# Kernel tuning notes

Measured on AMD Instinct MI355X. Metric: run time of the kernel, lower is better.

Reference implementation:

```python
import jax, jax.numpy as jnp
import numpy as np
import math

B, N, DQ, DK, DV, H = 8, 1024, 512, 512, 512, 8


def setup_inputs() -> dict:
    key = jax.random.key(0)
    ks = jax.random.split(key, 9)
    s = 0.02
    return {
        "Q": jax.random.normal(ks[0], (B, N, DQ), jnp.float32),
        "K": jax.random.normal(ks[1], (B, N, DK), jnp.float32),
        "mask": jax.random.bernoulli(ks[2], 0.9, (B, N)).astype(jnp.float32),
        "Wq": jax.random.normal(ks[3], (DQ, DV), jnp.float32) * s,
        "bq": jnp.zeros((DV,), jnp.float32),
        "Wk": jax.random.normal(ks[4], (DK, DV), jnp.float32) * s,
        "bk": jnp.zeros((DV,), jnp.float32),
        "Wv": jax.random.normal(ks[5], (DK, DV), jnp.float32) * s,
        "bv": jnp.zeros((DV,), jnp.float32),
        "Wo": jax.random.normal(ks[6], (DV, DV), jnp.float32) * s,
        "bo": jnp.zeros((DV,), jnp.float32),
    }


def reference(Q, K, mask, Wq, bq, Wk, bk, Wv, bv, Wo, bo):
    b, n, _ = Q.shape
    dV = Wq.shape[1]
    dh = dV // H
    scale = 1.0 / math.sqrt(dV)
    m = mask[..., None]                      # [B,N,1]
    Qp = (Q @ Wq + bq) * m                   # [B,N,dV]
    Kp = (K @ Wk + bk) * m
    Vp = (K @ Wv + bv) * m
    # torch.cat(x.split(dh,2),0) == head-major stacking -> keep as [H,B,N,dh]
    q = Qp.reshape(b, n, H, dh).transpose(2, 0, 1, 3)
    k = Kp.reshape(b, n, H, dh).transpose(2, 0, 1, 3)
    v = Vp.reshape(b, n, H, dh).transpose(2, 0, 1, 3)
    S = jnp.einsum('hbnd,hbmd->hbnm', q, k) * scale   # [H,B,N,N]
    mx = jnp.max(S, axis=3, keepdims=True)            # unmasked row max (faithful)
    m1 = mask[None, :, :, None]                       # [1,B,N,1]
    m2 = mask[None, :, None, :]                       # [1,B,1,N]
    num = jnp.exp((S - mx) * m1 * m2) * m1 * m2
    A = num / (jnp.sum(num, axis=3, keepdims=True) + 1e-16)
    O = q + jnp.einsum('hbnm,hbmd->hbnd', A, v)       # residual on Q_
    O = O.transpose(1, 2, 0, 3).reshape(b, n, dV)     # un-split heads
    O = O + jax.nn.relu((O @ Wo + bo) * m)
    return O
```

## Files before the change

kernel.cpp:

```cpp
#include <hip/hip_runtime.h>

typedef short bf16x8 __attribute__((ext_vector_type(8)));
typedef float f32x4 __attribute__((ext_vector_type(4)));

#define MFMA16(a, b, c) __builtin_amdgcn_mfma_f32_16x16x32_bf16((a), (b), (c), 0, 0, 0)

#define GLOAD_LDS16(g, l)                                              \
  __builtin_amdgcn_global_load_lds(                                    \
      (const __attribute__((address_space(1))) unsigned int*)(g),      \
      (__attribute__((address_space(3))) unsigned int*)(l), 16, 0, 0)

__device__ __forceinline__ unsigned short f2b(float f) {
  union { float f; unsigned int u; } x; x.f = f;
  unsigned int r = x.u + 0x7FFFu + ((x.u >> 16) & 1u);
  return (unsigned short)(r >> 16);
}
__device__ __forceinline__ float b2f(unsigned short h) {
  union { unsigned int u; float f; } x; x.u = ((unsigned int)h) << 16;
  return x.f;
}
__device__ __forceinline__ unsigned int cvtpk(float lo, float hi) {
  unsigned int r;
  asm("v_cvt_pk_bf16_f32 %0, %1, %2" : "=v"(r) : "v"(lo), "v"(hi));
  return r;
}

__global__ __launch_bounds__(256) void wtrans_kernel(
    const float* __restrict__ Wq, const float* __restrict__ Wk,
    const float* __restrict__ Wv, const float* __restrict__ Wo,
    short* __restrict__ Wt) {
  __shared__ float tile[64][65];
  const int z = blockIdx.z;
  const float* W = (z == 0) ? Wq : (z == 1) ? Wk : (z == 2) ? Wv : Wo;
  const int k0 = blockIdx.x * 64, n0 = blockIdx.y * 64;
  const int t = threadIdx.x;
  const int r = t >> 4, cc = (t & 15) * 4;
#pragma unroll
  for (int it = 0; it < 4; ++it) {
    int row = r + it * 16;
    const float4 v = *(const float4*)(W + (k0 + row) * 512 + n0 + cc);
    tile[row][cc + 0] = v.x; tile[row][cc + 1] = v.y;
    tile[row][cc + 2] = v.z; tile[row][cc + 3] = v.w;
  }
  __syncthreads();
  short* out = Wt + z * (512 * 512);
#pragma unroll
  for (int it = 0; it < 4; ++it) {
    int nrow = r + it * 16;
    unsigned int u0 = cvtpk(tile[cc + 0][nrow], tile[cc + 1][nrow]);
    unsigned int u1 = cvtpk(tile[cc + 2][nrow], tile[cc + 3][nrow]);
    uint2 uv; uv.x = u0; uv.y = u1;
    *(uint2*)(out + (n0 + nrow) * 512 + k0 + cc) = uv;
  }
}

__global__ __launch_bounds__(256) void cvt_kernel(
    const float* __restrict__ Q, const float* __restrict__ K,
    const float* __restrict__ mask,
    short* __restrict__ Qb, short* __restrict__ Kb, float* __restrict__ ml) {
  if (blockIdx.y == 0 && blockIdx.x < 4) {
    int i = (blockIdx.x * 256 + threadIdx.x) * 8;
    float4 a = *(const float4*)(mask + i);
    float4 bb = *(const float4*)(mask + i + 4);
    float4 ra, rb;
    ra.x = (a.x != 0.f) ? 0.f : -1e30f;
    ra.y = (a.y != 0.f) ? 0.f : -1e30f;
    ra.z = (a.z != 0.f) ? 0.f : -1e30f;
    ra.w = (a.w != 0.f) ? 0.f : -1e30f;
    rb.x = (bb.x != 0.f) ? 0.f : -1e30f;
    rb.y = (bb.y != 0.f) ? 0.f : -1e30f;
    rb.z = (bb.z != 0.f) ? 0.f : -1e30f;
    rb.w = (bb.w != 0.f) ? 0.f : -1e30f;
    *(float4*)(ml + i) = ra;
    *(float4*)(ml + i + 4) = rb;
  }
  const float* src = blockIdx.y ? K : Q;
  short* dst = blockIdx.y ? Kb : Qb;
  int i = (blockIdx.x * 256 + threadIdx.x) * 8;
  float4 v0 = *(const float4*)(src + i);
  float4 v1 = *(const float4*)(src + i + 4);
  uint2 a, b;
  a.x = cvtpk(v0.x, v0.y); a.y = cvtpk(v0.z, v0.w);
  b.x = cvtpk(v1.x, v1.y); b.y = cvtpk(v1.z, v1.w);
  *(uint2*)(dst + i) = a;
  *(uint2*)(dst + i + 4) = b;
}

__device__ __forceinline__ void gemm_bf16_core(
    const short* __restrict__ A, const short* __restrict__ Wt,
    short* Al, short* Bl, int m0, int t, f32x4 acc[4][4]) {
  const int lane = t & 63, w = t >> 6;
  const int c = lane & 15, g = lane >> 4;
  const int wr = w >> 1, wc = w & 1;
  const int lr = lane >> 3;
  const int sswz = ((lane & 7) ^ lr) << 3;
  const int swc = (c & 7) << 3;

  auto STAGE = [&](int kt, int buf) {
    short* Ad = Al + buf * 8192;
    short* Bd = Bl + buf * 8192;
#pragma unroll
    for (int it = 0; it < 4; ++it) {
      int row = w * 32 + it * 8;
      GLOAD_LDS16(A + (size_t)(m0 + row + lr) * 512 + kt * 64 + sswz, Ad + row * 64);
      GLOAD_LDS16(Wt + (size_t)(row + lr) * 512 + kt * 64 + sswz, Bd + row * 64);
    }
  };

  STAGE(0, 0);
  STAGE(1, 1);

  for (int kt = 0; kt < 8; ++kt) {
    if (kt < 7) { asm volatile("s_waitcnt vmcnt(8)" ::: "memory"); }
    else        { asm volatile("s_waitcnt vmcnt(0)" ::: "memory"); }
    __builtin_amdgcn_s_barrier();
    __builtin_amdgcn_sched_barrier(0);
    const short* Ac = Al + (kt & 1) * 8192;
    const short* Bc = Bl + (kt & 1) * 8192;
    __builtin_amdgcn_s_setprio(1);
#pragma unroll
    for (int kc = 0; kc < 2; ++kc) {
      bf16x8 af[4], bfr[4];
#pragma unroll
      for (int mi = 0; mi < 4; ++mi) {
        int r = wr * 64 + mi * 16 + c;
        af[mi] = *(const bf16x8*)(Ac + r * 64 + ((kc * 32 + 8 * g) ^ swc));
      }
#pragma unroll
      for (int ni = 0; ni < 4; ++ni) {
        int r = wc * 64 + ni * 16 + c;
        bfr[ni] = *(const bf16x8*)(Bc + r * 64 + ((kc * 32 + 8 * g) ^ swc));
      }
#pragma unroll
      for (int mi = 0; mi < 4; ++mi)
#pragma unroll
        for (int ni = 0; ni < 4; ++ni)
          acc[mi][ni] = MFMA16(af[mi], bfr[ni], acc[mi][ni]);
    }
    __builtin_amdgcn_s_setprio(0);
    __builtin_amdgcn_sched_barrier(0);
    __builtin_amdgcn_s_barrier();
    __builtin_amdgcn_sched_barrier(0);
    if (kt < 6) STAGE(kt + 2, kt & 1);
  }
}

__global__ __launch_bounds__(256) void proj2_kernel(
    const short* __restrict__ Qb, const short* __restrict__ Kb,
    const short* __restrict__ Wt4,
    const float* __restrict__ bq, const float* __restrict__ bk, const float* __restrict__ bv,
    const float* __restrict__ maskf,
    short* __restrict__ Qp, short* __restrict__ Kp, short* __restrict__ Vt) {
  __shared__ short Al[2 * 128 * 64];
  __shared__ short Bl[2 * 128 * 64];
  const int by = blockIdx.y;
  const int m0 = blockIdx.x * 128;
  const int t = threadIdx.x;
  const short* A;
  const short* Wt;
  const float* bias;
  int nbase;
  if (by < 4) { A = Qb; nbase = by * 128; Wt = Wt4 + nbase * 512; bias = bq; }
  else if (by < 8) { A = Kb; nbase = (by - 4) * 128; Wt = Wt4 + 262144 + nbase * 512; bias = bk; }
  else { A = Kb; nbase = (by - 8) * 128; Wt = Wt4 + 524288 + nbase * 512; bias = bv; }

  const f32x4 zz = {0.f, 0.f, 0.f, 0.f};
  f32x4 acc[4][4];
#pragma unroll
  for (int mi = 0; mi < 4; ++mi)
#pragma unroll
    for (int ni = 0; ni < 4; ++ni) acc[mi][ni] = zz;
  gemm_bf16_core(A, Wt, Al, Bl, m0, t, acc);

  const int lane = t & 63, w = t >> 6;
  const int c = lane & 15, g = lane >> 4;
  const int wr = w >> 1, wc = w & 1;
  float mk[4][4];
#pragma unroll
  for (int mi = 0; mi < 4; ++mi) {
    int mbase = m0 + wr * 64 + mi * 16 + 4 * g;
#pragma unroll
    for (int i = 0; i < 4; ++i) mk[mi][i] = maskf[mbase + i];
  }
  if (by < 8) {
    short* out = (by < 4) ? Qp : Kp;
#pragma unroll
    for (int ni = 0; ni < 4; ++ni) {
      int n = nbase + wc * 64 + ni * 16 + c;
      float bval = bias[n];
#pragma unroll
      for (int mi = 0; mi < 4; ++mi) {
        int mbase = m0 + wr * 64 + mi * 16 + 4 * g;
#pragma unroll
        for (int i = 0; i < 4; ++i)
          out[(size_t)(mbase + i) * 512 + n] = (short)f2b((acc[mi][ni][i] + bval) * mk[mi][i]);
      }
    }
  } else {
#pragma unroll
    for (int ni = 0; ni < 4; ++ni) {
      int d = nbase + wc * 64 + ni * 16 + c;
      int h = d >> 6, dd = d & 63;
      float bval = bias[d];
#pragma unroll
      for (int mi = 0; mi < 4; ++mi) {
        int mbase = m0 + wr * 64 + mi * 16 + 4 * g;
        int bi = mbase >> 10, seq0 = mbase & 1023;
        unsigned int u0 = cvtpk((acc[mi][ni][0] + bval) * mk[mi][0],
                                (acc[mi][ni][1] + bval) * mk[mi][1]);
        unsigned int u1 = cvtpk((acc[mi][ni][2] + bval) * mk[mi][2],
                                (acc[mi][ni][3] + bval) * mk[mi][3]);
        uint2 uv; uv.x = u0; uv.y = u1;
        *(uint2*)(Vt + ((size_t)(bi * 8 + h) * 64 + dd) * 1024 + seq0) = uv;
      }
    }
  }
}

__global__ __launch_bounds__(256) void attn_kernel(
    const short* __restrict__ Qp, const short* __restrict__ Kp,
    const short* __restrict__ Vt, const float* __restrict__ mask,
    const float* __restrict__ ml,
    float* __restrict__ Ob, short* __restrict__ Obb) {
  __shared__ short Kl[2][64][64];
  __shared__ short Vl[2][64][64];
  __shared__ short Pl[4][16][64];
  __shared__ float Mlds[1024];
  const int t = threadIdx.x, lane = t & 63, w = t >> 6;
  const int c = lane & 15, g = lane >> 4;
  const int hw = blockIdx.x;
  const int L = (hw & 7) * 128 + (hw >> 3);
  const int qt = L & 15, hb = L >> 4;
  const int b = hb & 7, h = hb >> 3;
  const int n0 = qt * 64;
  const float scale2 = 0.06375870724f;

  const short* Kg = Kp + (size_t)(b * 1024) * 512 + h * 64;
  const short* Vg = Vt + (size_t)((b * 8 + h) * 64) * 1024;
  const float* Lg = ml + b * 1024;
  const int srow = lane >> 3;
  const int sswz = ((lane & 7) ^ srow) << 3;
  const int r0 = w * 16, r1 = w * 16 + 8;
  const int swc = (c & 7) << 3;

  bf16x8 qf0, qf1;
  {
    const short* qptr = Qp + ((size_t)(b * 1024 + n0 + w * 16 + c) * 512 + h * 64 + 8 * g);
    qf0 = *(const bf16x8*)qptr;
    qf1 = *(const bf16x8*)(qptr + 32);
  }
  bf16x8 ones;
#pragma unroll
  for (int k = 0; k < 8; ++k) ones[k] = (short)0x3F80;

  auto STAGEKV = [&](int kvt, int buf) {
    const int kr = kvt * 64;
    GLOAD_LDS16(Kg + (size_t)(kr + r0 + srow) * 512 + sswz, &Kl[buf][r0][0]);
    GLOAD_LDS16(Kg + (size_t)(kr + r1 + srow) * 512 + sswz, &Kl[buf][r1][0]);
    GLOAD_LDS16(Vg + (size_t)(r0 + srow) * 1024 + kr + sswz, &Vl[buf][r0][0]);
    GLOAD_LDS16(Vg + (size_t)(r1 + srow) * 1024 + kr + sswz, &Vl[buf][r1][0]);
  };

  GLOAD_LDS16(Lg + w * 256 + lane * 4, &Mlds[w * 256]);
  STAGEKV(0, 0);
  STAGEKV(1, 1);

  const f32x4 zz = {0.f, 0.f, 0.f, 0.f};
  f32x4 o[4];
  o[0] = zz; o[1] = zz; o[2] = zz; o[3] = zz;
  f32x4 suma = zz;

#pragma unroll 1
  for (int kvt = 0; kvt < 16; ++kvt) {
    if (kvt < 15) { asm volatile("s_waitcnt vmcnt(4)" ::: "memory"); }
    else          { asm volatile("s_waitcnt vmcnt(0)" ::: "memory"); }
    __builtin_amdgcn_s_barrier();
    __builtin_amdgcn_sched_barrier(0);
    const int cur = kvt & 1;

    float4 lm[4];
#pragma unroll
    for (int j = 0; j < 4; ++j)
      lm[j] = *(const float4*)(&Mlds[kvt * 64 + 16 * j + 4 * g]);

    f32x4 s[4];
    __builtin_amdgcn_s_setprio(1);
#pragma unroll
    for (int j = 0; j < 4; ++j) {
      f32x4 sj = zz;
      sj = MFMA16(*(const bf16x8*)(&Kl[cur][16 * j + c][(8 * g) ^ swc]), qf0, sj);
      sj = MFMA16(*(const bf16x8*)(&Kl[cur][16 * j + c][(32 + 8 * g) ^ swc]), qf1, sj);
      s[j] = sj;
    }
    __builtin_amdgcn_s_setprio(0);

#pragma unroll
    for (int j = 0; j < 4; ++j) {
      float p0 = exp2f(fmaf(scale2, s[j][0], lm[j].x));
      float p1 = exp2f(fmaf(scale2, s[j][1], lm[j].y));
      float p2 = exp2f(fmaf(scale2, s[j][2], lm[j].z));
      float p3 = exp2f(fmaf(scale2, s[j][3], lm[j].w));
      uint2 pw; pw.x = cvtpk(p0, p1); pw.y = cvtpk(p2, p3);
      *(uint2*)(&Pl[w][c][(16 * j + 4 * g) ^ swc]) = pw;
    }

    __builtin_amdgcn_s_setprio(1);
#pragma unroll
    for (int ks = 0; ks < 2; ++ks) {
      bf16x8 pa = *(const bf16x8*)(&Pl[w][c][(ks * 32 + 8 * g) ^ swc]);
      suma = MFMA16(pa, ones, suma);
#pragma unroll
      for (int nb = 0; nb < 4; ++nb) {
        bf16x8 vb = *(const bf16x8*)(&Vl[cur][16 * nb + c][(ks * 32 + 8 * g) ^ swc]);
        o[nb] = MFMA16(pa, vb, o[nb]);
      }
    }
    __builtin_amdgcn_s_setprio(0);

    __builtin_amdgcn_sched_barrier(0);
    __builtin_amdgcn_s_barrier();
    __builtin_amdgcn_sched_barrier(0);
    if (kvt < 14) STAGEKV(kvt + 2, cur);
  }

  float inv[4], mk1[4];
#pragma unroll
  for (int i = 0; i < 4; ++i) {
    inv[i] = __builtin_amdgcn_rcpf(suma[i] + 1e-16f);
    mk1[i] = mask[b * 1024 + n0 + w * 16 + 4 * g + i];
  }
#pragma unroll
  for (int nb = 0; nb < 4; ++nb) {
    int colg = h * 64 + 16 * nb + c;
#pragma unroll
    for (int i = 0; i < 4; ++i) {
      int row = n0 + w * 16 + 4 * g + i;
      float att = o[nb][i] * inv[i];
      float qv = b2f(*(const unsigned short*)(Qp + (size_t)(b * 1024 + row) * 512 + colg));
      float res = qv + mk1[i] * att;
      size_t off = (size_t)(b * 1024 + row) * 512 + colg;
      Ob[off] = res;
      Obb[off] = (short)f2b(res);
    }
  }
}

__global__ __launch_bounds__(256) void final2_kernel(
    const short* __restrict__ Obb, const float* __restrict__ Obf,
    const short* __restrict__ Wto, const float* __restrict__ bo,
    const float* __restrict__ maskf, float* __restrict__ out) {
  __shared__ short Al[2 * 128 * 64];
  __shared__ short Bl[2 * 128 * 64];
  const int m0 = blockIdx.x * 128, n0 = blockIdx.y * 128;
  const int t = threadIdx.x;
  const f32x4 zz = {0.f, 0.f, 0.f, 0.f};
  f32x4 acc[4][4];
#pragma unroll
  for (int mi = 0; mi < 4; ++mi)
#pragma unroll
    for (int ni = 0; ni < 4; ++ni) acc[mi][ni] = zz;
  gemm_bf16_core(Obb, Wto + n0 * 512, Al, Bl, m0, t, acc);

  const int lane = t & 63, w = t >> 6;
  const int c = lane & 15, g = lane >> 4;
  const int wr = w >> 1, wc = w & 1;
  float mk[4][4];
#pragma unroll
  for (int mi = 0; mi < 4; ++mi) {
    int mbase = m0 + wr * 64 + mi * 16 + 4 * g;
#pragma unroll
    for (int i = 0; i < 4; ++i) mk[mi][i] = maskf[mbase + i];
  }
#pragma unroll
  for (int ni = 0; ni < 4; ++ni) {
    int n = n0 + wc * 64 + ni * 16 + c;
    float bval = bo[n];
#pragma unroll
    for (int mi = 0; mi < 4; ++mi) {
      int mbase = m0 + wr * 64 + mi * 16 + 4 * g;
#pragma unroll
      for (int i = 0; i < 4; ++i) {
        float v = (acc[mi][ni][i] + bval) * mk[mi][i];
        v = fmaxf(v, 0.f);
        size_t off = (size_t)(mbase + i) * 512 + n;
        out[off] = Obf[off] + v;
      }
    }
  }
}

extern "C" void kernel_launch(void* const* d_in, const int* in_sizes, int n_in,
                              void* d_out, int out_size, void* d_ws, size_t ws_size,
                              hipStream_t stream) {
  (void)in_sizes; (void)n_in; (void)ws_size;
  const float* Q    = (const float*)d_in[0];
  const float* K    = (const float*)d_in[1];
  const float* mask = (const float*)d_in[2];
  const float* Wq   = (const float*)d_in[3];
  const float* bq   = (const float*)d_in[4];
  const float* Wk   = (const float*)d_in[5];
  const float* bk   = (const float*)d_in[6];
  const float* Wv   = (const float*)d_in[7];
  const float* bv   = (const float*)d_in[8];
  const float* Wo   = (const float*)d_in[9];
  const float* bo   = (const float*)d_in[10];

  char* ws = (char*)d_ws;
  const size_t MB = 1048576;
  short* Wt4 = (short*)ws;
  short* Qb  = (short*)(ws + 2 * MB);
  short* Kb  = (short*)(ws + 10 * MB);
  short* Qp  = (short*)(ws + 18 * MB);
  short* Kp  = (short*)(ws + 26 * MB);
  short* Vt  = (short*)(ws + 34 * MB);
  short* Obb = (short*)(ws + 42 * MB);
  float* Ob  = (float*)(ws + 2 * MB);
  float* out = (float*)d_out;
  float* ml  = out + (out_size - 8192);

  wtrans_kernel<<<dim3(8, 8, 4), 256, 0, stream>>>(Wq, Wk, Wv, Wo, Wt4);
  cvt_kernel<<<dim3(2048, 2), 256, 0, stream>>>(Q, K, mask, Qb, Kb, ml);
  proj2_kernel<<<dim3(64, 12), 256, 0, stream>>>(Qb, Kb, Wt4, bq, bk, bv, mask, Qp, Kp, Vt);
  attn_kernel<<<dim3(1024), 256, 0, stream>>>(Qp, Kp, Vt, mask, ml, Ob, Obb);
  final2_kernel<<<dim3(64, 4), 256, 0, stream>>>(Obb, Ob, Wt4 + 3 * 262144, bo, mask, out);
}
```

Baseline: 98.82 us.

## Split attention KV range in two with separate combine kernel

Splits each attention tile's 1024-key range into two halves run by separate blocks (2048 blocks instead of 1024), writing unnormalized bf16 partial outputs and row sums, then adds a combine kernel that merges the halves, normalizes, adds the residual and writes bf16. The double-buffered async KV staging becomes single-buffered with full syncthreads, and the fp32 residual buffer is dropped so the final kernel reads the bf16 residual. This aims to raise parallelism and cut fp32 writes, at the cost of an extra launch, extra partial-result traffic, lost load/compute overlap and lower precision from bf16 partials and residual.

```diff
diff --git a/kernel.cpp b/kernel.cpp
--- a/kernel.cpp
+++ b/kernel.cpp
@@ -217,27 +217,32 @@
   }
 }
 
-__global__ __launch_bounds__(256) void attn_kernel(
+__global__ __launch_bounds__(256) void attn_split_kernel(
     const short* __restrict__ Qp, const short* __restrict__ Kp,
-    const short* __restrict__ Vt, const float* __restrict__ mask,
-    const float* __restrict__ ml,
-    float* __restrict__ Ob, short* __restrict__ Obb) {
-  __shared__ short Kl[2][64][64];
-  __shared__ short Vl[2][64][64];
+    const short* __restrict__ Vt, const float* __restrict__ ml,
+    short* __restrict__ OaccA, short* __restrict__ OaccB,
+    float* __restrict__ saccA, float* __restrict__ saccB) {
+  __shared__ short Kl[64][64];
+  __shared__ short Vl[64][64];
   __shared__ short Pl[4][16][64];
-  __shared__ float Mlds[1024];
+  __shared__ float Mlds[512];
   const int t = threadIdx.x, lane = t & 63, w = t >> 6;
   const int c = lane & 15, g = lane >> 4;
   const int hw = blockIdx.x;
-  const int L = (hw & 7) * 128 + (hw >> 3);
-  const int qt = L & 15, hb = L >> 4;
-  const int b = hb & 7, h = hb >> 3;
+  const int L = (hw & 7) * 256 + (hw >> 3);
+  const int head = L >> 5;
+  const int u = L & 31;
+  const int qt = u >> 1, s = u & 1;
+  const int b = head & 7, h = head >> 3;
   const int n0 = qt * 64;
   const float scale2 = 0.06375870724f;
 
-  const short* Kg = Kp + (size_t)(b * 1024) * 512 + h * 64;
-  const short* Vg = Vt + (size_t)((b * 8 + h) * 64) * 1024;
-  const float* Lg = ml + b * 1024;
+  const short* Kg = Kp + ((size_t)(b * 1024 + s * 512)) * 512 + h * 64;
+  const short* Vg = Vt + (size_t)((b * 8 + h) * 64) * 1024 + s * 512;
+  const float* Lg = ml + b * 1024 + s * 512;
+  short* OaccS = s ? OaccB : OaccA;
+  float* saccS = s ? saccB : saccA;
+
   const int srow = lane >> 3;
   const int sswz = ((lane & 7) ^ srow) << 3;
   const int r0 = w * 16, r1 = w * 16 + 8;
@@ -253,17 +258,17 @@
 #pragma unroll
   for (int k = 0; k < 8; ++k) ones[k] = (short)0x3F80;
 
-  auto STAGEKV = [&](int kvt, int buf) {
+  auto STAGEKV = [&](int kvt) {
     const int kr = kvt * 64;
-    GLOAD_LDS16(Kg + (size_t)(kr + r0 + srow) * 512 + sswz, &Kl[buf][r0][0]);
-    GLOAD_LDS16(Kg + (size_t)(kr + r1 + srow) * 512 + sswz, &Kl[buf][r1][0]);
-    GLOAD_LDS16(Vg + (size_t)(r0 + srow) * 1024 + kr + sswz, &Vl[buf][r0][0]);
-    GLOAD_LDS16(Vg + (size_t)(r1 + srow) * 1024 + kr + sswz, &Vl[buf][r1][0]);
+    GLOAD_LDS16(Kg + (size_t)(kr + r0 + srow) * 512 + sswz, &Kl[r0][0]);
+    GLOAD_LDS16(Kg + (size_t)(kr + r1 + srow) * 512 + sswz, &Kl[r1][0]);
+    GLOAD_LDS16(Vg + (size_t)(r0 + srow) * 1024 + kr + sswz, &Vl[r0][0]);
+    GLOAD_LDS16(Vg + (size_t)(r1 + srow) * 1024 + kr + sswz, &Vl[r1][0]);
   };
 
-  GLOAD_LDS16(Lg + w * 256 + lane * 4, &Mlds[w * 256]);
-  STAGEKV(0, 0);
-  STAGEKV(1, 1);
+  if (w < 2) GLOAD_LDS16(Lg + w * 256 + lane * 4, &Mlds[w * 256]);
+  STAGEKV(0);
+  __syncthreads();
 
   const f32x4 zz = {0.f, 0.f, 0.f, 0.f};
   f32x4 o[4];
@@ -271,35 +276,29 @@
   f32x4 suma = zz;
 
 #pragma unroll 1
-  for (int kvt = 0; kvt < 16; ++kvt) {
-    if (kvt < 15) { asm volatile("s_waitcnt vmcnt(4)" ::: "memory"); }
-    else          { asm volatile("s_waitcnt vmcnt(0)" ::: "memory"); }
-    __builtin_amdgcn_s_barrier();
-    __builtin_amdgcn_sched_barrier(0);
-    const int cur = kvt & 1;
-
+  for (int kvt = 0; kvt < 8; ++kvt) {
     float4 lm[4];
 #pragma unroll
     for (int j = 0; j < 4; ++j)
       lm[j] = *(const float4*)(&Mlds[kvt * 64 + 16 * j + 4 * g]);
 
-    f32x4 s[4];
+    f32x4 sv[4];
     __builtin_amdgcn_s_setprio(1);
 #pragma unroll
     for (int j = 0; j < 4; ++j) {
       f32x4 sj = zz;
-      sj = MFMA16(*(const bf16x8*)(&Kl[cur][16 * j + c][(8 * g) ^ swc]), qf0, sj);
-      sj = MFMA16(*(const bf16x8*)(&Kl[cur][16 * j + c][(32 + 8 * g) ^ swc]), qf1, sj);
-      s[j] = sj;
+      sj = MFMA16(*(const bf16x8*)(&Kl[16 * j + c][(8 * g) ^ swc]), qf0, sj);
+      sj = MFMA16(*(const bf16x8*)(&Kl[16 * j + c][(32 + 8 * g) ^ swc]), qf1, sj);
+      sv[j] = sj;
     }
     __builtin_amdgcn_s_setprio(0);
 
 #pragma unroll
     for (int j = 0; j < 4; ++j) {
-      float p0 = exp2f(fmaf(scale2, s[j][0], lm[j].x));
-      float p1 = exp2f(fmaf(scale2, s[j][1], lm[j].y));
-      float p2 = exp2f(fmaf(scale2, s[j][2], lm[j].z));
-      float p3 = exp2f(fmaf(scale2, s[j][3], lm[j].w));
+      float p0 = exp2f(fmaf(scale2, sv[j][0], lm[j].x));
+      float p1 = exp2f(fmaf(scale2, sv[j][1], lm[j].y));
+      float p2 = exp2f(fmaf(scale2, sv[j][2], lm[j].z));
+      float p3 = exp2f(fmaf(scale2, sv[j][3], lm[j].w));
       uint2 pw; pw.x = cvtpk(p0, p1); pw.y = cvtpk(p2, p3);
       *(uint2*)(&Pl[w][c][(16 * j + 4 * g) ^ swc]) = pw;
     }
@@ -311,42 +310,65 @@
       suma = MFMA16(pa, ones, suma);
 #pragma unroll
       for (int nb = 0; nb < 4; ++nb) {
-        bf16x8 vb = *(const bf16x8*)(&Vl[cur][16 * nb + c][(ks * 32 + 8 * g) ^ swc]);
+        bf16x8 vb = *(const bf16x8*)(&Vl[16 * nb + c][(ks * 32 + 8 * g) ^ swc]);
         o[nb] = MFMA16(pa, vb, o[nb]);
       }
     }
     __builtin_amdgcn_s_setprio(0);
 
-    __builtin_amdgcn_sched_barrier(0);
-    __builtin_amdgcn_s_barrier();
-    __builtin_amdgcn_sched_barrier(0);
-    if (kvt < 14) STAGEKV(kvt + 2, cur);
-  }
-
-  float inv[4], mk1[4];
-#pragma unroll
-  for (int i = 0; i < 4; ++i) {
-    inv[i] = __builtin_amdgcn_rcpf(suma[i] + 1e-16f);
-    mk1[i] = mask[b * 1024 + n0 + w * 16 + 4 * g + i];
-  }
+    if (kvt < 7) {
+      __syncthreads();
+      STAGEKV(kvt + 1);
+      __syncthreads();
+    }
+  }
+
 #pragma unroll
   for (int nb = 0; nb < 4; ++nb) {
     int colg = h * 64 + 16 * nb + c;
 #pragma unroll
     for (int i = 0; i < 4; ++i) {
       int row = n0 + w * 16 + 4 * g + i;
-      float att = o[nb][i] * inv[i];
-      float qv = b2f(*(const unsigned short*)(Qp + (size_t)(b * 1024 + row) * 512 + colg));
-      float res = qv + mk1[i] * att;
-      size_t off = (size_t)(b * 1024 + row) * 512 + colg;
-      Ob[off] = res;
-      Obb[off] = (short)f2b(res);
-    }
-  }
+      OaccS[(size_t)(b * 1024 + row) * 512 + colg] = (short)f2b(o[nb][i]);
+    }
+  }
+  if (c == 0) {
+#pragma unroll
+    for (int i = 0; i < 4; ++i) {
+      int row = n0 + w * 16 + 4 * g + i;
+      saccS[(size_t)(b * 1024 + row) * 8 + h] = suma[i];
+    }
+  }
+}
+
+__global__ __launch_bounds__(256) void combine_kernel(
+    const short* __restrict__ OaccA, const short* __restrict__ OaccB,
+    const float* __restrict__ saccA, const float* __restrict__ saccB,
+    const short* __restrict__ Qp, const float* __restrict__ mask,
+    short* __restrict__ Obb) {
+  const int e = (blockIdx.x * 256 + threadIdx.x) * 8;
+  const int row = e >> 9;
+  const int h = (e & 511) >> 6;
+  const float sA = saccA[row * 8 + h], sB = saccB[row * 8 + h];
+  const float inv = __builtin_amdgcn_rcpf(sA + sB + 1e-16f);
+  const float mk = mask[row];
+  bf16x8 a = *(const bf16x8*)(OaccA + e);
+  bf16x8 bb = *(const bf16x8*)(OaccB + e);
+  bf16x8 q = *(const bf16x8*)(Qp + e);
+  float r[8];
+#pragma unroll
+  for (int k = 0; k < 8; ++k) {
+    float num = b2f((unsigned short)a[k]) + b2f((unsigned short)bb[k]);
+    r[k] = b2f((unsigned short)q[k]) + mk * (num * inv);
+  }
+  uint4 rr;
+  rr.x = cvtpk(r[0], r[1]); rr.y = cvtpk(r[2], r[3]);
+  rr.z = cvtpk(r[4], r[5]); rr.w = cvtpk(r[6], r[7]);
+  *(uint4*)(Obb + e) = rr;
 }
 
 __global__ __launch_bounds__(256) void final2_kernel(
-    const short* __restrict__ Obb, const float* __restrict__ Obf,
+    const short* __restrict__ Obb,
     const short* __restrict__ Wto, const float* __restrict__ bo,
     const float* __restrict__ maskf, float* __restrict__ out) {
   __shared__ short Al[2 * 128 * 64];
@@ -383,7 +405,7 @@
         float v = (acc[mi][ni][i] + bval) * mk[mi][i];
         v = fmaxf(v, 0.f);
         size_t off = (size_t)(mbase + i) * 512 + n;
-        out[off] = Obf[off] + v;
+        out[off] = b2f((unsigned short)Obb[off]) + v;
       }
     }
   }
@@ -392,7 +414,7 @@
 extern "C" void kernel_launch(void* const* d_in, const int* in_sizes, int n_in,
                               void* d_out, int out_size, void* d_ws, size_t ws_size,
                               hipStream_t stream) {
-  (void)in_sizes; (void)n_in; (void)ws_size;
+  (void)in_sizes; (void)n_in; (void)out_size; (void)ws_size;
   const float* Q    = (const float*)d_in[0];
   const float* K    = (const float*)d_in[1];
   const float* mask = (const float*)d_in[2];
@@ -407,20 +429,24 @@
 
   char* ws = (char*)d_ws;
   const size_t MB = 1048576;
-  short* Wt4 = (short*)ws;
-  short* Qb  = (short*)(ws + 2 * MB);
-  short* Kb  = (short*)(ws + 10 * MB);
-  short* Qp  = (short*)(ws + 18 * MB);
-  short* Kp  = (short*)(ws + 26 * MB);
-  short* Vt  = (short*)(ws + 34 * MB);
-  short* Obb = (short*)(ws + 42 * MB);
-  float* Ob  = (float*)(ws + 2 * MB);
-  float* out = (float*)d_out;
-  float* ml  = out + (out_size - 8192);
+  short* Wt4   = (short*)ws;
+  short* Qb    = (short*)(ws + 2 * MB);
+  short* Kb    = (short*)(ws + 10 * MB);
+  short* OaccA = (short*)(ws + 2 * MB);
+  short* OaccB = (short*)(ws + 10 * MB);
+  short* Qp    = (short*)(ws + 18 * MB);
+  short* Kp    = (short*)(ws + 26 * MB);
+  short* Vt    = (short*)(ws + 34 * MB);
+  short* Obb   = (short*)(ws + 42 * MB);
+  float* ml    = (float*)(ws + 50 * MB);
+  float* saccA = (float*)(ws + 50 * MB + 262144);
+  float* saccB = (float*)(ws + 50 * MB + 2 * 262144);
+  float* out   = (float*)d_out;
 
   wtrans_kernel<<<dim3(8, 8, 4), 256, 0, stream>>>(Wq, Wk, Wv, Wo, Wt4);
   cvt_kernel<<<dim3(2048, 2), 256, 0, stream>>>(Q, K, mask, Qb, Kb, ml);
   proj2_kernel<<<dim3(64, 12), 256, 0, stream>>>(Qb, Kb, Wt4, bq, bk, bv, mask, Qp, Kp, Vt);
-  attn_kernel<<<dim3(1024), 256, 0, stream>>>(Qp, Kp, Vt, mask, ml, Ob, Obb);
-  final2_kernel<<<dim3(64, 4), 256, 0, stream>>>(Obb, Ob, Wt4 + 3 * 262144, bo, mask, out);
-}
+  attn_split_kernel<<<dim3(2048), 256, 0, stream>>>(Qp, Kp, Vt, ml, OaccA, OaccB, saccA, saccB);
+  combine_kernel<<<dim3(2048), 256, 0, stream>>>(OaccA, OaccB, saccA, saccB, Qp, mask, Obb);
+  final2_kernel<<<dim3(64, 4), 256, 0, stream>>>(Obb, Wt4 + 3 * 262144, bo, mask, out);
+}
```

Measured after the change: 95.94 us. 1.03x faster.
